# Performance work log

Measured on AMD Instinct MI355X. Metric: run time of the kernel, lower is better.

The kernel has to match this reference:

```python
import jax, jax.numpy as jnp
import numpy as np

EPS = 1e-5


def _linear(x, w, b):
    # torch Linear: y = x @ w.T + b, w shape [out, in]
    return x @ w.T + b


def _batchnorm(x, gamma, beta):
    # training-mode BatchNorm1d: per-feature batch stats, biased variance
    m = jnp.mean(x, axis=0)
    v = jnp.var(x, axis=0)
    return (x - m) * jax.lax.rsqrt(v + EPS) * gamma + beta


def _noise_like(key, x):
    # mimics: mean = x.mean().item(); std = x.std().item() * U(1,2);
    # noise ~ N(mean, std) of x.shape, detached.
    ku, kn = jax.random.split(key)
    m = jax.lax.stop_gradient(jnp.mean(x))
    s = jax.lax.stop_gradient(jnp.std(x, ddof=1))
    u = jax.random.uniform(ku, (), dtype=x.dtype, minval=1.0, maxval=2.0)
    return m + s * u * jax.random.normal(kn, x.shape, dtype=x.dtype)


def setup_inputs() -> dict:
    key = jax.random.key(0)
    ks = jax.random.split(key, 12)
    B = 65536
    x = jax.random.normal(ks[0], (B, 784), dtype=jnp.float32)

    def lin_init(kw, kb, fan_in, fan_out):
        bound = 1.0 / np.sqrt(fan_in)
        w = jax.random.uniform(kw, (fan_out, fan_in), minval=-bound, maxval=bound, dtype=jnp.float32)
        b = jax.random.uniform(kb, (fan_out,), minval=-bound, maxval=bound, dtype=jnp.float32)
        return w, b

    w1, b1 = lin_init(ks[1], ks[2], 784, 48)
    w2, b2 = lin_init(ks[3], ks[4], 48, 24)
    w3, b3 = lin_init(ks[5], ks[6], 24, 10)
    return {
        "x": x,
        "w1": w1, "b1": b1,
        "gamma1": jnp.ones((48,), jnp.float32), "beta1": jnp.zeros((48,), jnp.float32),
        "w2": w2, "b2": b2,
        "gamma2": jnp.ones((24,), jnp.float32), "beta2": jnp.zeros((24,), jnp.float32),
        "w3": w3, "b3": b3,
    }


def reference(x, w1, b1, gamma1, beta1, w2, b2, gamma2, beta2, w3, b3):
    k1 = jax.random.key(1234)
    k2 = jax.random.key(5678)
    h = _batchnorm(_linear(x, w1, b1), gamma1, beta1)
    h = h + _noise_like(k1, h)
    h = jax.nn.relu(h)
    h = _batchnorm(_linear(h, w2, b2), gamma2, beta2)
    h = h + _noise_like(k2, h)
    h = jax.nn.relu(h)
    return _linear(h, w3, b3)
```

## Files before the change

kernel.cpp:

```cpp
#include <hip/hip_runtime.h>
#include <cstdint>
#include <cstring>


constexpr int MROWS = 65536;
constexpr int KDIM  = 784;
constexpr int KPAD  = 800;
constexpr int F1 = 48, F2 = 24, F3 = 10;

using frag_ab = __attribute__((ext_vector_type(8))) short;
using frag_cd = __attribute__((ext_vector_type(4))) float;

union UB { uint4 u; frag_ab f; };

__device__ __forceinline__ uint32_t rotl32(uint32_t v, int r) {
  return (v << r) | (v >> (32 - r));
}

__device__ __forceinline__ uint32_t tf_mix(uint32_t k0, uint32_t k1, uint32_t ctr) {
  uint32_t ks2 = k0 ^ k1 ^ 0x1BD11BDAu;
  uint32_t x0 = k0;
  uint32_t x1 = ctr + k1;
#define TFR(r) { x0 += x1; x1 = rotl32(x1, r); x1 ^= x0; }
  TFR(13) TFR(15) TFR(26) TFR(6)
  x0 += k1;  x1 += ks2 + 1u;
  TFR(17) TFR(29) TFR(16) TFR(24)
  x0 += ks2; x1 += k0 + 2u;
  TFR(13) TFR(15) TFR(26) TFR(6)
  x0 += k0;  x1 += k1 + 3u;
  TFR(17) TFR(29) TFR(16) TFR(24)
  x0 += k1;  x1 += ks2 + 4u;
  TFR(13) TFR(15) TFR(26) TFR(6)
  x0 += ks2; x1 += k0 + 5u;
#undef TFR
  return x0 ^ x1;
}

__device__ __forceinline__ float erfinv_f32(float x) {
  float t = fmaxf(1.0f - x * x, 1.0e-30f);
  float w = -__logf(t);
  float p;
  if (w < 5.0f) {
    w = w - 2.5f;
    p = 2.81022636e-08f;
    p = fmaf(p, w, 3.43273939e-07f);
    p = fmaf(p, w, -3.5233877e-06f);
    p = fmaf(p, w, -4.39150654e-06f);
    p = fmaf(p, w, 0.00021858087f);
    p = fmaf(p, w, -0.00125372503f);
    p = fmaf(p, w, -0.00417768164f);
    p = fmaf(p, w, 0.246640727f);
    p = fmaf(p, w, 1.50140941f);
  } else {
    w = sqrtf(w) - 3.0f;
    p = -0.000200214257f;
    p = fmaf(p, w, 0.000100950558f);
    p = fmaf(p, w, 0.00134934322f);
    p = fmaf(p, w, -0.00367342844f);
    p = fmaf(p, w, 0.00573950773f);
    p = fmaf(p, w, -0.0076224613f);
    p = fmaf(p, w, 0.00943887047f);
    p = fmaf(p, w, 1.00167406f);
    p = fmaf(p, w, 2.83297682f);
  }
  return p * x;
}

__device__ __forceinline__ float noise_normal(uint32_t k0, uint32_t k1, uint32_t ctr) {
  uint32_t bits = tf_mix(k0, k1, ctr);
  float f = __uint_as_float((bits >> 9) | 0x3f800000u) - 1.0f;
  const float lo = -0.99999994f;
  float u = fmaxf(lo, f * 2.0f + lo);
  return 1.41421356f * erfinv_f32(u);
}

__device__ __forceinline__ uint32_t pkbf(float a, float b) {
  uint32_t ua = __float_as_uint(a); ua += 0x7fffu + ((ua >> 16) & 1u);
  uint32_t ub = __float_as_uint(b); ub += 0x7fffu + ((ub >> 16) & 1u);
  return (ua >> 16) | (ub & 0xffff0000u);
}

__device__ __forceinline__ uint32_t cvtpk(float a, float b) {
  uint32_t r;
  asm("v_cvt_pk_bf16_f32 %0, %1, %2" : "=v"(r) : "v"(a), "v"(b));
  return r;
}

__global__ void k_prep(const float* __restrict__ w1, ushort* __restrict__ wb1,
                       float* __restrict__ st) {
  int i = blockIdx.x * 256 + threadIdx.x;
  if (i < 2048) st[i] = 0.f;
  if (i >= F1 * KPAD) return;
  int n = i / KPAD, k = i - n * KPAD;
  float v = (k < KDIM) ? w1[n * KDIM + k] : 0.f;
  uint32_t u = __float_as_uint(v);
  u += 0x7fffu + ((u >> 16) & 1u);
  wb1[i] = (ushort)(u >> 16);
}

__global__ __launch_bounds__(256, 4) void k_gemm1(
    const float* __restrict__ x, const ushort* __restrict__ wb1,
    const float* __restrict__ b1, float* __restrict__ h1,
    float* __restrict__ fsum, float* __restrict__ fssq) {
  __shared__ float reds[4][48], redq[4][48];

  const int t = threadIdx.x;
  const int w = t >> 6;
  const int l = t & 63;
  const int lane16 = l & 15;
  const int quad = l >> 4;
  const int rowbase = blockIdx.x * 64;
  const int myrow = rowbase + w * 16 + lane16;

  frag_cd acc[3];
#pragma unroll
  for (int ct = 0; ct < 3; ++ct)
#pragma unroll
    for (int r = 0; r < 4; ++r) acc[ct][r] = 0.f;

  const float* ap = x + (size_t)myrow * KDIM + quad * 8;
  const ushort* bp0 = wb1 + (size_t)(0 * 16 + lane16) * KPAD + quad * 8;
  const ushort* bp1 = wb1 + (size_t)(1 * 16 + lane16) * KPAD + quad * 8;
  const ushort* bp2 = wb1 + (size_t)(2 * 16 + lane16) * KPAD + quad * 8;

  float4 ca0 = *(const float4*)(ap);
  float4 ca1 = *(const float4*)(ap + 4);
  uint4 cb0 = *(const uint4*)(bp0);
  uint4 cb1 = *(const uint4*)(bp1);
  uint4 cb2 = *(const uint4*)(bp2);

  for (int s = 0; s < 25; ++s) {
    float4 na0 = make_float4(0.f, 0.f, 0.f, 0.f);
    float4 na1 = na0;
    uint4 nb0 = make_uint4(0, 0, 0, 0), nb1 = nb0, nb2 = nb0;
    if (s < 24) {
      const int ko = (s + 1) * 32;
      if (ko + quad * 8 + 8 <= KDIM) {
        na0 = *(const float4*)(ap + ko);
        na1 = *(const float4*)(ap + ko + 4);
      }
      nb0 = *(const uint4*)(bp0 + ko);
      nb1 = *(const uint4*)(bp1 + ko);
      nb2 = *(const uint4*)(bp2 + ko);
    }
    UB a;
    a.u.x = cvtpk(ca0.x, ca0.y);
    a.u.y = cvtpk(ca0.z, ca0.w);
    a.u.z = cvtpk(ca1.x, ca1.y);
    a.u.w = cvtpk(ca1.z, ca1.w);
    UB b;
    b.u = cb0; acc[0] = __builtin_amdgcn_mfma_f32_16x16x32_bf16(a.f, b.f, acc[0], 0, 0, 0);
    b.u = cb1; acc[1] = __builtin_amdgcn_mfma_f32_16x16x32_bf16(a.f, b.f, acc[1], 0, 0, 0);
    b.u = cb2; acc[2] = __builtin_amdgcn_mfma_f32_16x16x32_bf16(a.f, b.f, acc[2], 0, 0, 0);
    ca0 = na0; ca1 = na1; cb0 = nb0; cb1 = nb1; cb2 = nb2;
  }

  float bias[3];
#pragma unroll
  for (int ct = 0; ct < 3; ++ct) bias[ct] = b1[ct * 16 + lane16];
  float psum[3] = {0.f, 0.f, 0.f}, pssq[3] = {0.f, 0.f, 0.f};
#pragma unroll
  for (int r = 0; r < 4; ++r) {
    const int grow = rowbase + w * 16 + quad * 4 + r;
#pragma unroll
    for (int ct = 0; ct < 3; ++ct) {
      float v = acc[ct][r] + bias[ct];
      h1[(size_t)grow * F1 + ct * 16 + lane16] = v;
      psum[ct] += v;
      pssq[ct] += v * v;
    }
  }
#pragma unroll
  for (int ct = 0; ct < 3; ++ct) {
    psum[ct] += __shfl_xor(psum[ct], 16, 64);
    psum[ct] += __shfl_xor(psum[ct], 32, 64);
    pssq[ct] += __shfl_xor(pssq[ct], 16, 64);
    pssq[ct] += __shfl_xor(pssq[ct], 32, 64);
  }
  if (quad == 0) {
#pragma unroll
    for (int ct = 0; ct < 3; ++ct) {
      reds[w][ct * 16 + lane16] = psum[ct];
      redq[w][ct * 16 + lane16] = pssq[ct];
    }
  }
  __syncthreads();
  if (t < F1) {
    float s = reds[0][t] + reds[1][t] + reds[2][t] + reds[3][t];
    float q = redq[0][t] + redq[1][t] + redq[2][t] + redq[3][t];
    const int rep = blockIdx.x & 7;
    atomicAdd(&fsum[rep * 48 + t], s);
    atomicAdd(&fssq[rep * 48 + t], q);
  }
}

__global__ __launch_bounds__(256) void k_layer2(
    const float* __restrict__ h1, const float* __restrict__ w2,
    const float* __restrict__ b2, const float* __restrict__ gamma1,
    const float* __restrict__ beta1, const float* __restrict__ fsum,
    const float* __restrict__ fssq, float u1,
    float* __restrict__ h2, float* __restrict__ fsum2, float* __restrict__ fssq2,
    uint32_t kna, uint32_t knb) {
  __shared__ float a1s[64][49];
  __shared__ float w2s[48][25];
  __shared__ float h2s[64][25];
  __shared__ float bnp[4][48];
  __shared__ float scal[2];

  const int t = threadIdx.x;
  const int rowbase = blockIdx.x * 64;

  float cm = 0.f, cs = 0.f;
  if (t < F1) {
    float s0 = 0.f, q0 = 0.f;
#pragma unroll
    for (int rp = 0; rp < 8; ++rp) { s0 += fsum[rp * 48 + t]; q0 += fssq[rp * 48 + t]; }
    float m = s0 * (1.f / 65536.f);
    float v = q0 * (1.f / 65536.f) - m * m;
    float r = rsqrtf(v + 1e-5f);
    float g = gamma1[t], b = beta1[t];
    bnp[0][t] = m; bnp[1][t] = r; bnp[2][t] = g; bnp[3][t] = b;
    cm = b;
    cs = g * g * r * r * v + b * b;
  }
  if (t < 64) {
#pragma unroll
    for (int off = 32; off > 0; off >>= 1) {
      cm += __shfl_down(cm, off, 64);
      cs += __shfl_down(cs, off, 64);
    }
    if (t == 0) {
      float m = cm / (float)F1;
      float SS = 65536.f * cs;
      float Ntot = 65536.f * (float)F1;
      float s2 = (SS - Ntot * m * m) / (Ntot - 1.f);
      scal[0] = m;
      scal[1] = sqrtf(s2) * u1;
    }
  }
  for (int e = t; e < F2 * 48; e += 256) {
    int c = e / 48, k = e - c * 48;
    w2s[k][c] = w2[e];
  }
  __syncthreads();
  const float m1 = scal[0], su1 = scal[1];

  const int rr = t >> 2;
  const int cc0 = (t & 3) * 12;
  const int grow = rowbase + rr;
  const float* hrow = h1 + (size_t)grow * F1 + cc0;
#pragma unroll
  for (int jj = 0; jj < 12; jj += 4) {
    float4 hv = *(const float4*)(hrow + jj);
    float vv[4] = {hv.x, hv.y, hv.z, hv.w};
#pragma unroll
    for (int q = 0; q < 4; ++q) {
      int c = cc0 + jj + q;
      float bn = (vv[q] - bnp[0][c]) * bnp[1][c] * bnp[2][c] + bnp[3][c];
      uint32_t ctr = (uint32_t)grow * 48u + (uint32_t)c;
      float nz = noise_normal(kna, knb, ctr);
      float val = bn + fmaf(su1, nz, m1);
      a1s[rr][c] = fmaxf(val, 0.f);
    }
  }
  __syncthreads();

  const int rr2 = t & 63;
  const int c0 = (t >> 6) * 6;
  float acc[6] = {0.f, 0.f, 0.f, 0.f, 0.f, 0.f};
#pragma unroll
  for (int k = 0; k < 48; ++k) {
    float a = a1s[rr2][k];
#pragma unroll
    for (int j = 0; j < 6; ++j)
      acc[j] = fmaf(a, w2s[k][c0 + j], acc[j]);
  }
#pragma unroll
  for (int j = 0; j < 6; ++j)
    h2s[rr2][c0 + j] = acc[j] + b2[c0 + j];
  __syncthreads();

  for (int e = t; e < 64 * F2; e += 256) {
    int r2 = e / 24, c2 = e - r2 * 24;
    h2[(size_t)rowbase * F2 + e] = h2s[r2][c2];
  }
  if (t < F2) {
    float s = 0.f, q = 0.f;
    for (int r2 = 0; r2 < 64; ++r2) {
      float v = h2s[r2][t];
      s += v; q += v * v;
    }
    const int rep = blockIdx.x & 7;
    atomicAdd(&fsum2[rep * 24 + t], s);
    atomicAdd(&fssq2[rep * 24 + t], q);
  }
}

__global__ __launch_bounds__(256) void k_layer3(
    const float* __restrict__ h2, const float* __restrict__ w3,
    const float* __restrict__ b3, const float* __restrict__ gamma2,
    const float* __restrict__ beta2, const float* __restrict__ fsum2,
    const float* __restrict__ fssq2, float u2,
    float* __restrict__ out, uint32_t kna, uint32_t knb) {
  __shared__ float a2s[64][25];
  __shared__ float w3s[24][10];
  __shared__ float bnp[4][24];
  __shared__ float scal[2];

  const int t = threadIdx.x;
  const int rowbase = blockIdx.x * 64;

  float cm = 0.f, cs = 0.f;
  if (t < F2) {
    float s0 = 0.f, q0 = 0.f;
#pragma unroll
    for (int rp = 0; rp < 8; ++rp) { s0 += fsum2[rp * 24 + t]; q0 += fssq2[rp * 24 + t]; }
    float m = s0 * (1.f / 65536.f);
    float v = q0 * (1.f / 65536.f) - m * m;
    float r = rsqrtf(v + 1e-5f);
    float g = gamma2[t], b = beta2[t];
    bnp[0][t] = m; bnp[1][t] = r; bnp[2][t] = g; bnp[3][t] = b;
    cm = b;
    cs = g * g * r * r * v + b * b;
  }
  if (t < 64) {
#pragma unroll
    for (int off = 32; off > 0; off >>= 1) {
      cm += __shfl_down(cm, off, 64);
      cs += __shfl_down(cs, off, 64);
    }
    if (t == 0) {
      float m = cm / (float)F2;
      float SS = 65536.f * cs;
      float Ntot = 65536.f * (float)F2;
      float s2 = (SS - Ntot * m * m) / (Ntot - 1.f);
      scal[0] = m;
      scal[1] = sqrtf(s2) * u2;
    }
  }
  if (t < F3 * F2) {
    int c = t / 24, k = t - c * 24;
    w3s[k][c] = w3[t];
  }
  __syncthreads();
  const float m2 = scal[0], su2 = scal[1];

  for (int e = t; e < 64 * F2; e += 256) {
    int r = e / 24, c = e - r * 24;
    float v = h2[(size_t)rowbase * F2 + e];
    float bn = (v - bnp[0][c]) * bnp[1][c] * bnp[2][c] + bnp[3][c];
    uint32_t ctr = (uint32_t)(rowbase * F2 + e);
    float nz = noise_normal(kna, knb, ctr);
    float val = bn + fmaf(su2, nz, m2);
    a2s[r][c] = fmaxf(val, 0.f);
  }
  __syncthreads();

  if (t < 128) {
    const int rr = t & 63;
    const int c0 = (t >> 6) * 5;
    float acc[5] = {0.f, 0.f, 0.f, 0.f, 0.f};
#pragma unroll
    for (int k = 0; k < 24; ++k) {
      float a = a2s[rr][k];
#pragma unroll
      for (int j = 0; j < 5; ++j)
        acc[j] = fmaf(a, w3s[k][c0 + j], acc[j]);
    }
    size_t ob = (size_t)(rowbase + rr) * F3 + c0;
#pragma unroll
    for (int j = 0; j < 5; ++j) out[ob + j] = acc[j] + b3[c0 + j];
  }
}

static void host_tf(uint32_t k0, uint32_t k1, uint32_t c0, uint32_t c1,
                    uint32_t& o0, uint32_t& o1) {
  uint32_t ks2 = k0 ^ k1 ^ 0x1BD11BDAu;
  uint32_t x0 = c0 + k0, x1 = c1 + k1;
  auto R = [&](int r) { x0 += x1; x1 = (x1 << r) | (x1 >> (32 - r)); x1 ^= x0; };
  R(13); R(15); R(26); R(6);  x0 += k1;  x1 += ks2 + 1u;
  R(17); R(29); R(16); R(24); x0 += ks2; x1 += k0 + 2u;
  R(13); R(15); R(26); R(6);  x0 += k0;  x1 += k1 + 3u;
  R(17); R(29); R(16); R(24); x0 += k1;  x1 += ks2 + 4u;
  R(13); R(15); R(26); R(6);  x0 += ks2; x1 += k0 + 5u;
  o0 = x0; o1 = x1;
}

static float host_uniform12(uint32_t seed) {
  uint32_t ka, kb, t0, t1;
  host_tf(0u, seed, 0u, 0u, ka, kb);
  host_tf(ka, kb, 0u, 0u, t0, t1);
  uint32_t bits = t0 ^ t1;
  uint32_t fb = (bits >> 9) | 0x3f800000u;
  float f;
  std::memcpy(&f, &fb, 4);
  return f;
}

extern "C" void kernel_launch(void* const* d_in, const int* in_sizes, int n_in,
                              void* d_out, int out_size, void* d_ws, size_t ws_size,
                              hipStream_t stream) {
  (void)in_sizes; (void)n_in; (void)out_size; (void)ws_size;
  const float* x      = (const float*)d_in[0];
  const float* w1     = (const float*)d_in[1];
  const float* b1     = (const float*)d_in[2];
  const float* gamma1 = (const float*)d_in[3];
  const float* beta1  = (const float*)d_in[4];
  const float* w2     = (const float*)d_in[5];
  const float* b2     = (const float*)d_in[6];
  const float* gamma2 = (const float*)d_in[7];
  const float* beta2  = (const float*)d_in[8];
  const float* w3     = (const float*)d_in[9];
  const float* b3     = (const float*)d_in[10];
  float* out = (float*)d_out;

  float* h1 = (float*)d_ws;
  float* h2 = h1 + (size_t)MROWS * F1;
  float* st = h2 + (size_t)MROWS * F2;
  ushort* wb1 = (ushort*)(st + 2048);

  uint32_t kn1a, kn1b, kn2a, kn2b;
  host_tf(0u, 1234u, 0u, 1u, kn1a, kn1b);
  host_tf(0u, 5678u, 0u, 1u, kn2a, kn2b);
  float u1 = host_uniform12(1234u);
  float u2 = host_uniform12(5678u);

  k_prep<<<(F1 * KPAD + 255) / 256, 256, 0, stream>>>(w1, wb1, st);
  k_gemm1<<<MROWS / 64, 256, 0, stream>>>(x, wb1, b1, h1, st + 0, st + 384);
  k_layer2<<<MROWS / 64, 256, 0, stream>>>(h1, w2, b2, gamma1, beta1,
                                           st + 0, st + 384, u1,
                                           h2, st + 768, st + 960, kn1a, kn1b);
  k_layer3<<<MROWS / 64, 256, 0, stream>>>(h2, w3, b3, gamma2, beta2,
                                           st + 768, st + 960, u2,
                                           out, kn2a, kn2b);
}
```

Measured before the change: 78.01 us.

## Stage x tiles through double-buffered swizzled LDS with coalesced loads in GEMM1

GEMM1 previously had each lane load its own strided 32-byte pieces of x directly into MFMA fragments. Now each block cooperatively loads 128-column chunks of x with row-contiguous float4 loads into a double-buffered, XOR-swizzled shared-memory tile, then reads the A fragments from LDS. The 16-column tail is handled separately. The aim is better coalescing of the dominant x read and overlap of global loads with MFMA work, at the cost of 64KB of LDS per block (launch bounds lowered to 2) and extra barriers.

```diff
diff --git a/kernel.cpp b/kernel.cpp
--- a/kernel.cpp
+++ b/kernel.cpp
@@ -7,6 +7,7 @@
 constexpr int KDIM  = 784;
 constexpr int KPAD  = 800;
 constexpr int F1 = 48, F2 = 24, F3 = 10;
+constexpr int NBLK = 1024;
 
 using frag_ab = __attribute__((ext_vector_type(8))) short;
 using frag_cd = __attribute__((ext_vector_type(4))) float;
@@ -74,12 +75,6 @@
   return 1.41421356f * erfinv_f32(u);
 }
 
-__device__ __forceinline__ uint32_t pkbf(float a, float b) {
-  uint32_t ua = __float_as_uint(a); ua += 0x7fffu + ((ua >> 16) & 1u);
-  uint32_t ub = __float_as_uint(b); ub += 0x7fffu + ((ub >> 16) & 1u);
-  return (ua >> 16) | (ub & 0xffff0000u);
-}
-
 __device__ __forceinline__ uint32_t cvtpk(float a, float b) {
   uint32_t r;
   asm("v_cvt_pk_bf16_f32 %0, %1, %2" : "=v"(r) : "v"(a), "v"(b));
@@ -98,10 +93,11 @@
   wb1[i] = (ushort)(u >> 16);
 }
 
-__global__ __launch_bounds__(256, 4) void k_gemm1(
+__global__ __launch_bounds__(256, 2) void k_gemm1(
     const float* __restrict__ x, const ushort* __restrict__ wb1,
     const float* __restrict__ b1, float* __restrict__ h1,
     float* __restrict__ fsum, float* __restrict__ fssq) {
+  __shared__ float xs[2][64 * 128];
   __shared__ float reds[4][48], redq[4][48];
 
   const int t = threadIdx.x;
@@ -112,47 +108,96 @@
   const int rowbase = blockIdx.x * 64;
   const int myrow = rowbase + w * 16 + lane16;
 
+  const int sr = t >> 2;
+  const int sq = t & 3;
+  const float* srcrow = x + (size_t)(rowbase + sr) * KDIM + sq * 32;
+  const int swz = sr & 15;
+
   frag_cd acc[3];
 #pragma unroll
   for (int ct = 0; ct < 3; ++ct)
 #pragma unroll
     for (int r = 0; r < 4; ++r) acc[ct][r] = 0.f;
 
-  const float* ap = x + (size_t)myrow * KDIM + quad * 8;
   const ushort* bp0 = wb1 + (size_t)(0 * 16 + lane16) * KPAD + quad * 8;
   const ushort* bp1 = wb1 + (size_t)(1 * 16 + lane16) * KPAD + quad * 8;
   const ushort* bp2 = wb1 + (size_t)(2 * 16 + lane16) * KPAD + quad * 8;
 
-  float4 ca0 = *(const float4*)(ap);
-  float4 ca1 = *(const float4*)(ap + 4);
-  uint4 cb0 = *(const uint4*)(bp0);
-  uint4 cb1 = *(const uint4*)(bp1);
-  uint4 cb2 = *(const uint4*)(bp2);
-
-  for (int s = 0; s < 25; ++s) {
-    float4 na0 = make_float4(0.f, 0.f, 0.f, 0.f);
-    float4 na1 = na0;
-    uint4 nb0 = make_uint4(0, 0, 0, 0), nb1 = nb0, nb2 = nb0;
-    if (s < 24) {
-      const int ko = (s + 1) * 32;
-      if (ko + quad * 8 + 8 <= KDIM) {
-        na0 = *(const float4*)(ap + ko);
-        na1 = *(const float4*)(ap + ko + 4);
+  const int ardbase = (w * 16 + lane16) * 128;
+
+  {
+    float4 stg[8];
+#pragma unroll
+    for (int j = 0; j < 8; ++j) stg[j] = *(const float4*)(srcrow + j * 4);
+#pragma unroll
+    for (int j = 0; j < 8; ++j) {
+      int sp = sq * 8 + j;
+      *(float4*)&xs[0][sr * 128 + ((sp ^ swz) << 2)] = stg[j];
+    }
+  }
+  __syncthreads();
+
+  int buf = 0;
+  for (int c = 0; c < 6; ++c) {
+    uint4 b0[4], b1[4], b2[4];
+#pragma unroll
+    for (int ks = 0; ks < 4; ++ks) {
+      const int ko = c * 128 + ks * 32;
+      b0[ks] = *(const uint4*)(bp0 + ko);
+      b1[ks] = *(const uint4*)(bp1 + ko);
+      b2[ks] = *(const uint4*)(bp2 + ko);
+    }
+    float4 stg[8];
+    if (c < 5) {
+#pragma unroll
+      for (int j = 0; j < 8; ++j)
+        stg[j] = *(const float4*)(srcrow + (c + 1) * 128 + j * 4);
+    }
+#pragma unroll
+    for (int ks = 0; ks < 4; ++ks) {
+      const int sp0 = ks * 8 + quad * 2;
+      float4 a0 = *(const float4*)&xs[buf][ardbase + ((sp0 ^ lane16) << 2)];
+      float4 a1 = *(const float4*)&xs[buf][ardbase + (((sp0 + 1) ^ lane16) << 2)];
+      UB a;
+      a.u.x = cvtpk(a0.x, a0.y);
+      a.u.y = cvtpk(a0.z, a0.w);
+      a.u.z = cvtpk(a1.x, a1.y);
+      a.u.w = cvtpk(a1.z, a1.w);
+      UB b;
+      b.u = b0[ks]; acc[0] = __builtin_amdgcn_mfma_f32_16x16x32_bf16(a.f, b.f, acc[0], 0, 0, 0);
+      b.u = b1[ks]; acc[1] = __builtin_amdgcn_mfma_f32_16x16x32_bf16(a.f, b.f, acc[1], 0, 0, 0);
+      b.u = b2[ks]; acc[2] = __builtin_amdgcn_mfma_f32_16x16x32_bf16(a.f, b.f, acc[2], 0, 0, 0);
+    }
+    if (c < 5) {
+#pragma unroll
+      for (int j = 0; j < 8; ++j) {
+        int sp = sq * 8 + j;
+        *(float4*)&xs[buf ^ 1][sr * 128 + ((sp ^ swz) << 2)] = stg[j];
       }
-      nb0 = *(const uint4*)(bp0 + ko);
-      nb1 = *(const uint4*)(bp1 + ko);
-      nb2 = *(const uint4*)(bp2 + ko);
-    }
+    }
+    __syncthreads();
+    buf ^= 1;
+  }
+
+  {
+    float4 a0 = make_float4(0.f, 0.f, 0.f, 0.f), a1 = a0;
+    if (quad < 2) {
+      const float* apt = x + (size_t)myrow * KDIM + 768 + quad * 8;
+      a0 = *(const float4*)(apt);
+      a1 = *(const float4*)(apt + 4);
+    }
+    uint4 tb0 = *(const uint4*)(bp0 + 768);
+    uint4 tb1 = *(const uint4*)(bp1 + 768);
+    uint4 tb2 = *(const uint4*)(bp2 + 768);
     UB a;
-    a.u.x = cvtpk(ca0.x, ca0.y);
-    a.u.y = cvtpk(ca0.z, ca0.w);
-    a.u.z = cvtpk(ca1.x, ca1.y);
-    a.u.w = cvtpk(ca1.z, ca1.w);
+    a.u.x = cvtpk(a0.x, a0.y);
+    a.u.y = cvtpk(a0.z, a0.w);
+    a.u.z = cvtpk(a1.x, a1.y);
+    a.u.w = cvtpk(a1.z, a1.w);
     UB b;
-    b.u = cb0; acc[0] = __builtin_amdgcn_mfma_f32_16x16x32_bf16(a.f, b.f, acc[0], 0, 0, 0);
-    b.u = cb1; acc[1] = __builtin_amdgcn_mfma_f32_16x16x32_bf16(a.f, b.f, acc[1], 0, 0, 0);
-    b.u = cb2; acc[2] = __builtin_amdgcn_mfma_f32_16x16x32_bf16(a.f, b.f, acc[2], 0, 0, 0);
-    ca0 = na0; ca1 = na1; cb0 = nb0; cb1 = nb1; cb2 = nb2;
+    b.u = tb0; acc[0] = __builtin_amdgcn_mfma_f32_16x16x32_bf16(a.f, b.f, acc[0], 0, 0, 0);
+    b.u = tb1; acc[1] = __builtin_amdgcn_mfma_f32_16x16x32_bf16(a.f, b.f, acc[1], 0, 0, 0);
+    b.u = tb2; acc[2] = __builtin_amdgcn_mfma_f32_16x16x32_bf16(a.f, b.f, acc[2], 0, 0, 0);
   }
 
   float bias[3];
@@ -426,11 +471,11 @@
   float u2 = host_uniform12(5678u);
 
   k_prep<<<(F1 * KPAD + 255) / 256, 256, 0, stream>>>(w1, wb1, st);
-  k_gemm1<<<MROWS / 64, 256, 0, stream>>>(x, wb1, b1, h1, st + 0, st + 384);
-  k_layer2<<<MROWS / 64, 256, 0, stream>>>(h1, w2, b2, gamma1, beta1,
-                                           st + 0, st + 384, u1,
-                                           h2, st + 768, st + 960, kn1a, kn1b);
-  k_layer3<<<MROWS / 64, 256, 0, stream>>>(h2, w3, b3, gamma2, beta2,
-                                           st + 768, st + 960, u2,
-                                           out, kn2a, kn2b);
-}
+  k_gemm1<<<NBLK, 256, 0, stream>>>(x, wb1, b1, h1, st + 0, st + 384);
+  k_layer2<<<NBLK, 256, 0, stream>>>(h1, w2, b2, gamma1, beta1,
+                                     st + 0, st + 384, u1,
+                                     h2, st + 768, st + 960, kn1a, kn1b);
+  k_layer3<<<NBLK, 256, 0, stream>>>(h2, w3, b3, gamma2, beta2,
+                                     st + 768, st + 960, u2,
+                                     out, kn2a, kn2b);
+}
```

After: 83.12 us. 1.07x slower.

## Stage x tiles through LDS with coalesced loads and drop the weight-prep kernel

Applied to the files above, without the earlier changes.

The first GEMM now loads x with row-contiguous float4 loads: 16 lanes cover 64 consecutive floats of one row. The data goes into a double-buffered LDS tile, from which each lane reads its MFMA A-fragment, replacing strided per-lane row loads straight from global memory. The separate k_prep kernel that converted w1 to padded bf16 is removed, so each block reads fp32 w1 directly and packs it to bf16 in the loop, with a dedicated tail step for the last 16 columns. Stat buffers are now zeroed with hipMemsetAsync. This trades one launch and better x coalescing for redundant weight conversion work in every block and more LDS traffic.

```diff
diff --git a/kernel.cpp b/kernel.cpp
--- a/kernel.cpp
+++ b/kernel.cpp
@@ -5,8 +5,8 @@
 
 constexpr int MROWS = 65536;
 constexpr int KDIM  = 784;
-constexpr int KPAD  = 800;
 constexpr int F1 = 48, F2 = 24, F3 = 10;
+constexpr int NBLK = 1024;
 
 using frag_ab = __attribute__((ext_vector_type(8))) short;
 using frag_cd = __attribute__((ext_vector_type(4))) float;
@@ -74,34 +74,26 @@
   return 1.41421356f * erfinv_f32(u);
 }
 
-__device__ __forceinline__ uint32_t pkbf(float a, float b) {
-  uint32_t ua = __float_as_uint(a); ua += 0x7fffu + ((ua >> 16) & 1u);
-  uint32_t ub = __float_as_uint(b); ub += 0x7fffu + ((ub >> 16) & 1u);
-  return (ua >> 16) | (ub & 0xffff0000u);
-}
-
 __device__ __forceinline__ uint32_t cvtpk(float a, float b) {
   uint32_t r;
   asm("v_cvt_pk_bf16_f32 %0, %1, %2" : "=v"(r) : "v"(a), "v"(b));
   return r;
 }
 
-__global__ void k_prep(const float* __restrict__ w1, ushort* __restrict__ wb1,
-                       float* __restrict__ st) {
-  int i = blockIdx.x * 256 + threadIdx.x;
-  if (i < 2048) st[i] = 0.f;
-  if (i >= F1 * KPAD) return;
-  int n = i / KPAD, k = i - n * KPAD;
-  float v = (k < KDIM) ? w1[n * KDIM + k] : 0.f;
-  uint32_t u = __float_as_uint(v);
-  u += 0x7fffu + ((u >> 16) & 1u);
-  wb1[i] = (ushort)(u >> 16);
+__device__ __forceinline__ frag_ab packfrag(float4 a0, float4 a1) {
+  UB a;
+  a.u.x = cvtpk(a0.x, a0.y);
+  a.u.y = cvtpk(a0.z, a0.w);
+  a.u.z = cvtpk(a1.x, a1.y);
+  a.u.w = cvtpk(a1.z, a1.w);
+  return a.f;
 }
 
 __global__ __launch_bounds__(256, 4) void k_gemm1(
-    const float* __restrict__ x, const ushort* __restrict__ wb1,
+    const float* __restrict__ x, const float* __restrict__ w1,
     const float* __restrict__ b1, float* __restrict__ h1,
     float* __restrict__ fsum, float* __restrict__ fssq) {
+  __shared__ float xs[2][64][68];
   __shared__ float reds[4][48], redq[4][48];
 
   const int t = threadIdx.x;
@@ -118,41 +110,85 @@
 #pragma unroll
     for (int r = 0; r < 4; ++r) acc[ct][r] = 0.f;
 
-  const float* ap = x + (size_t)myrow * KDIM + quad * 8;
-  const ushort* bp0 = wb1 + (size_t)(0 * 16 + lane16) * KPAD + quad * 8;
-  const ushort* bp1 = wb1 + (size_t)(1 * 16 + lane16) * KPAD + quad * 8;
-  const ushort* bp2 = wb1 + (size_t)(2 * 16 + lane16) * KPAD + quad * 8;
-
-  float4 ca0 = *(const float4*)(ap);
-  float4 ca1 = *(const float4*)(ap + 4);
-  uint4 cb0 = *(const uint4*)(bp0);
-  uint4 cb1 = *(const uint4*)(bp1);
-  uint4 cb2 = *(const uint4*)(bp2);
-
-  for (int s = 0; s < 25; ++s) {
-    float4 na0 = make_float4(0.f, 0.f, 0.f, 0.f);
-    float4 na1 = na0;
-    uint4 nb0 = make_uint4(0, 0, 0, 0), nb1 = nb0, nb2 = nb0;
-    if (s < 24) {
-      const int ko = (s + 1) * 32;
-      if (ko + quad * 8 + 8 <= KDIM) {
-        na0 = *(const float4*)(ap + ko);
-        na1 = *(const float4*)(ap + ko + 4);
-      }
-      nb0 = *(const uint4*)(bp0 + ko);
-      nb1 = *(const uint4*)(bp1 + ko);
-      nb2 = *(const uint4*)(bp2 + ko);
-    }
-    UB a;
-    a.u.x = cvtpk(ca0.x, ca0.y);
-    a.u.y = cvtpk(ca0.z, ca0.w);
-    a.u.z = cvtpk(ca1.x, ca1.y);
-    a.u.w = cvtpk(ca1.z, ca1.w);
-    UB b;
-    b.u = cb0; acc[0] = __builtin_amdgcn_mfma_f32_16x16x32_bf16(a.f, b.f, acc[0], 0, 0, 0);
-    b.u = cb1; acc[1] = __builtin_amdgcn_mfma_f32_16x16x32_bf16(a.f, b.f, acc[1], 0, 0, 0);
-    b.u = cb2; acc[2] = __builtin_amdgcn_mfma_f32_16x16x32_bf16(a.f, b.f, acc[2], 0, 0, 0);
-    ca0 = na0; ca1 = na1; cb0 = nb0; cb1 = nb1; cb2 = nb2;
+  const int sro = (l >> 4);
+  const int scol = (l & 15) * 4;
+  const float* sbase = x + (size_t)(rowbase + w * 16 + sro) * KDIM + scol;
+  const int lrow = w * 16 + sro;
+
+  const float* wp0 = w1 + (size_t)lane16 * KDIM + quad * 8;
+  const float* wp1 = wp0 + (size_t)16 * KDIM;
+  const float* wp2 = wp0 + (size_t)32 * KDIM;
+
+  const float* arow = &xs[0][w * 16 + lane16][0];
+  const int xsstride = 64 * 68;
+
+  float4 sg0, sg1, sg2, sg3;
+
+  sg0 = *(const float4*)(sbase);
+  sg1 = *(const float4*)(sbase + 4 * KDIM);
+  sg2 = *(const float4*)(sbase + 8 * KDIM);
+  sg3 = *(const float4*)(sbase + 12 * KDIM);
+  *(float4*)&xs[0][lrow][scol] = sg0;
+  *(float4*)&xs[0][lrow + 4][scol] = sg1;
+  *(float4*)&xs[0][lrow + 8][scol] = sg2;
+  *(float4*)&xs[0][lrow + 12][scol] = sg3;
+
+#define MFMA_STEP(bufidx, koff)                                                 \
+  {                                                                             \
+    float4 b0a = *(const float4*)(wp0 + (koff));                                \
+    float4 b0b = *(const float4*)(wp0 + (koff) + 4);                            \
+    float4 b1a = *(const float4*)(wp1 + (koff));                                \
+    float4 b1b = *(const float4*)(wp1 + (koff) + 4);                            \
+    float4 b2a = *(const float4*)(wp2 + (koff));                                \
+    float4 b2b = *(const float4*)(wp2 + (koff) + 4);                            \
+    const float* ar = arow + (bufidx) * xsstride + ((koff) & 63) + quad * 8;    \
+    float4 a0 = *(const float4*)(ar);                                           \
+    float4 a1 = *(const float4*)(ar + 4);                                       \
+    frag_ab af = packfrag(a0, a1);                                              \
+    acc[0] = __builtin_amdgcn_mfma_f32_16x16x32_bf16(af, packfrag(b0a, b0b), acc[0], 0, 0, 0); \
+    acc[1] = __builtin_amdgcn_mfma_f32_16x16x32_bf16(af, packfrag(b1a, b1b), acc[1], 0, 0, 0); \
+    acc[2] = __builtin_amdgcn_mfma_f32_16x16x32_bf16(af, packfrag(b2a, b2b), acc[2], 0, 0, 0); \
+  }
+
+  int buf = 0;
+  for (int c = 0; c < 11; ++c) {
+    const int cn = (c + 1) * 64;
+    sg0 = *(const float4*)(sbase + cn);
+    sg1 = *(const float4*)(sbase + cn + 4 * KDIM);
+    sg2 = *(const float4*)(sbase + cn + 8 * KDIM);
+    sg3 = *(const float4*)(sbase + cn + 12 * KDIM);
+    MFMA_STEP(buf, c * 64)
+    MFMA_STEP(buf, c * 64 + 32)
+    *(float4*)&xs[buf ^ 1][lrow][scol] = sg0;
+    *(float4*)&xs[buf ^ 1][lrow + 4][scol] = sg1;
+    *(float4*)&xs[buf ^ 1][lrow + 8][scol] = sg2;
+    *(float4*)&xs[buf ^ 1][lrow + 12][scol] = sg3;
+    buf ^= 1;
+  }
+  float4 ta0 = make_float4(0.f, 0.f, 0.f, 0.f), ta1 = ta0;
+  if (quad < 2) {
+    const float* apt = x + (size_t)myrow * KDIM + 768 + quad * 8;
+    ta0 = *(const float4*)(apt);
+    ta1 = *(const float4*)(apt + 4);
+  }
+  MFMA_STEP(buf, 11 * 64)
+  MFMA_STEP(buf, 11 * 64 + 32)
+#undef MFMA_STEP
+  {
+    float4 b0a = ta0, b0b = ta0, b1a = ta0, b1b = ta0, b2a = ta0, b2b = ta0;
+    b0a = b0b = b1a = b1b = b2a = b2b = make_float4(0.f, 0.f, 0.f, 0.f);
+    if (quad < 2) {
+      b0a = *(const float4*)(wp0 + 768);
+      b0b = *(const float4*)(wp0 + 772);
+      b1a = *(const float4*)(wp1 + 768);
+      b1b = *(const float4*)(wp1 + 772);
+      b2a = *(const float4*)(wp2 + 768);
+      b2b = *(const float4*)(wp2 + 772);
+    }
+    frag_ab af = packfrag(ta0, ta1);
+    acc[0] = __builtin_amdgcn_mfma_f32_16x16x32_bf16(af, packfrag(b0a, b0b), acc[0], 0, 0, 0);
+    acc[1] = __builtin_amdgcn_mfma_f32_16x16x32_bf16(af, packfrag(b1a, b1b), acc[1], 0, 0, 0);
+    acc[2] = __builtin_amdgcn_mfma_f32_16x16x32_bf16(af, packfrag(b2a, b2b), acc[2], 0, 0, 0);
   }
 
   float bias[3];
@@ -417,7 +453,6 @@
   float* h1 = (float*)d_ws;
   float* h2 = h1 + (size_t)MROWS * F1;
   float* st = h2 + (size_t)MROWS * F2;
-  ushort* wb1 = (ushort*)(st + 2048);
 
   uint32_t kn1a, kn1b, kn2a, kn2b;
   host_tf(0u, 1234u, 0u, 1u, kn1a, kn1b);
@@ -425,12 +460,12 @@
   float u1 = host_uniform12(1234u);
   float u2 = host_uniform12(5678u);
 
-  k_prep<<<(F1 * KPAD + 255) / 256, 256, 0, stream>>>(w1, wb1, st);
-  k_gemm1<<<MROWS / 64, 256, 0, stream>>>(x, wb1, b1, h1, st + 0, st + 384);
-  k_layer2<<<MROWS / 64, 256, 0, stream>>>(h1, w2, b2, gamma1, beta1,
-                                           st + 0, st + 384, u1,
-                                           h2, st + 768, st + 960, kn1a, kn1b);
-  k_layer3<<<MROWS / 64, 256, 0, stream>>>(h2, w3, b3, gamma2, beta2,
-                                           st + 768, st + 960, u2,
-                                           out, kn2a, kn2b);
-}
+  hipMemsetAsync(st, 0, 2048 * sizeof(float), stream);
+  k_gemm1<<<NBLK, 256, 0, stream>>>(x, w1, b1, h1, st + 0, st + 384);
+  k_layer2<<<NBLK, 256, 0, stream>>>(h1, w2, b2, gamma1, beta1,
+                                     st + 0, st + 384, u1,
+                                     h2, st + 768, st + 960, kn1a, kn1b);
+  k_layer3<<<NBLK, 256, 0, stream>>>(h2, w3, b3, gamma2, beta2,
+                                     st + 768, st + 960, u2,
+                                     out, kn2a, kn2b);
+}
```

Result: slower. 91.95 us (+17.9%).

## Stage x tiles through double-buffered LDS with coalesced loads in GEMM1

Applied to the files above, without the earlier changes.

GEMM1 now loads contiguous 64-column strips of x per wave with fully coalesced float4 reads. It writes them into a padded, double-buffered shared-memory tile and reads MFMA A-fragments from LDS, while prefetching the next strip and the weight fragments. The 16-column tail is handled separately from global memory. This removes the strided per-lane row reads of the old loop, at the cost of extra LDS traffic and more registers. It relies on intra-wave ordering rather than barriers.

```diff
diff --git a/kernel.cpp b/kernel.cpp
--- a/kernel.cpp
+++ b/kernel.cpp
@@ -7,6 +7,8 @@
 constexpr int KDIM  = 784;
 constexpr int KPAD  = 800;
 constexpr int F1 = 48, F2 = 24, F3 = 10;
+constexpr int NBLK = 1024;
+constexpr int XP   = 68;
 
 using frag_ab = __attribute__((ext_vector_type(8))) short;
 using frag_cd = __attribute__((ext_vector_type(4))) float;
@@ -74,16 +76,19 @@
   return 1.41421356f * erfinv_f32(u);
 }
 
-__device__ __forceinline__ uint32_t pkbf(float a, float b) {
-  uint32_t ua = __float_as_uint(a); ua += 0x7fffu + ((ua >> 16) & 1u);
-  uint32_t ub = __float_as_uint(b); ub += 0x7fffu + ((ub >> 16) & 1u);
-  return (ua >> 16) | (ub & 0xffff0000u);
-}
-
 __device__ __forceinline__ uint32_t cvtpk(float a, float b) {
   uint32_t r;
   asm("v_cvt_pk_bf16_f32 %0, %1, %2" : "=v"(r) : "v"(a), "v"(b));
   return r;
+}
+
+__device__ __forceinline__ frag_ab packfrag(float4 a0, float4 a1) {
+  UB a;
+  a.u.x = cvtpk(a0.x, a0.y);
+  a.u.y = cvtpk(a0.z, a0.w);
+  a.u.z = cvtpk(a1.x, a1.y);
+  a.u.w = cvtpk(a1.z, a1.w);
+  return a.f;
 }
 
 __global__ void k_prep(const float* __restrict__ w1, ushort* __restrict__ wb1,
@@ -102,6 +107,7 @@
     const float* __restrict__ x, const ushort* __restrict__ wb1,
     const float* __restrict__ b1, float* __restrict__ h1,
     float* __restrict__ fsum, float* __restrict__ fssq) {
+  __shared__ float xs[2][64][XP];
   __shared__ float reds[4][48], redq[4][48];
 
   const int t = threadIdx.x;
@@ -118,42 +124,108 @@
 #pragma unroll
     for (int r = 0; r < 4; ++r) acc[ct][r] = 0.f;
 
-  const float* ap = x + (size_t)myrow * KDIM + quad * 8;
-  const ushort* bp0 = wb1 + (size_t)(0 * 16 + lane16) * KPAD + quad * 8;
-  const ushort* bp1 = wb1 + (size_t)(1 * 16 + lane16) * KPAD + quad * 8;
-  const ushort* bp2 = wb1 + (size_t)(2 * 16 + lane16) * KPAD + quad * 8;
-
-  float4 ca0 = *(const float4*)(ap);
-  float4 ca1 = *(const float4*)(ap + 4);
-  uint4 cb0 = *(const uint4*)(bp0);
-  uint4 cb1 = *(const uint4*)(bp1);
-  uint4 cb2 = *(const uint4*)(bp2);
-
-  for (int s = 0; s < 25; ++s) {
-    float4 na0 = make_float4(0.f, 0.f, 0.f, 0.f);
-    float4 na1 = na0;
-    uint4 nb0 = make_uint4(0, 0, 0, 0), nb1 = nb0, nb2 = nb0;
-    if (s < 24) {
-      const int ko = (s + 1) * 32;
-      if (ko + quad * 8 + 8 <= KDIM) {
-        na0 = *(const float4*)(ap + ko);
-        na1 = *(const float4*)(ap + ko + 4);
-      }
-      nb0 = *(const uint4*)(bp0 + ko);
-      nb1 = *(const uint4*)(bp1 + ko);
-      nb2 = *(const uint4*)(bp2 + ko);
-    }
-    UB a;
-    a.u.x = cvtpk(ca0.x, ca0.y);
-    a.u.y = cvtpk(ca0.z, ca0.w);
-    a.u.z = cvtpk(ca1.x, ca1.y);
-    a.u.w = cvtpk(ca1.z, ca1.w);
+  const int sro = l >> 4;
+  const int scol = (l & 15) * 4;
+  const float* sbase = x + (size_t)(rowbase + w * 16 + sro) * KDIM + scol;
+  float* lw0 = &xs[0][w * 16 + sro][scol];
+  float* lw1 = &xs[1][w * 16 + sro][scol];
+
+  const ushort* bp0 = wb1 + (size_t)lane16 * KPAD + quad * 8;
+  const ushort* bp1 = bp0 + 16 * KPAD;
+  const ushort* bp2 = bp0 + 32 * KPAD;
+
+  const float* ar0 = &xs[0][w * 16 + lane16][quad * 8];
+  const float* ar1 = &xs[1][w * 16 + lane16][quad * 8];
+
+#define LOADC(R0, R1, R2, R3, ko)                                \
+  {                                                              \
+    R0 = *(const float4*)(sbase + (ko));                         \
+    R1 = *(const float4*)(sbase + (ko) + 4 * KDIM);              \
+    R2 = *(const float4*)(sbase + (ko) + 8 * KDIM);              \
+    R3 = *(const float4*)(sbase + (ko) + 12 * KDIM);             \
+  }
+#define WRITEC(DST, R0, R1, R2, R3)                              \
+  {                                                              \
+    *(float4*)((DST)) = R0;                                      \
+    *(float4*)((DST) + 4 * XP) = R1;                             \
+    *(float4*)((DST) + 8 * XP) = R2;                             \
+    *(float4*)((DST) + 12 * XP) = R3;                            \
+  }
+#define COMPUTE2(AR, Q0, Q1, Q2, Q3, Q4, Q5)                                      \
+  {                                                                               \
+    frag_ab af = packfrag(*(const float4*)(AR), *(const float4*)((AR) + 4));      \
+    UB b;                                                                         \
+    b.u = Q0; acc[0] = __builtin_amdgcn_mfma_f32_16x16x32_bf16(af, b.f, acc[0], 0, 0, 0); \
+    b.u = Q1; acc[1] = __builtin_amdgcn_mfma_f32_16x16x32_bf16(af, b.f, acc[1], 0, 0, 0); \
+    b.u = Q2; acc[2] = __builtin_amdgcn_mfma_f32_16x16x32_bf16(af, b.f, acc[2], 0, 0, 0); \
+    af = packfrag(*(const float4*)((AR) + 32), *(const float4*)((AR) + 36));      \
+    b.u = Q3; acc[0] = __builtin_amdgcn_mfma_f32_16x16x32_bf16(af, b.f, acc[0], 0, 0, 0); \
+    b.u = Q4; acc[1] = __builtin_amdgcn_mfma_f32_16x16x32_bf16(af, b.f, acc[1], 0, 0, 0); \
+    b.u = Q5; acc[2] = __builtin_amdgcn_mfma_f32_16x16x32_bf16(af, b.f, acc[2], 0, 0, 0); \
+  }
+
+  float4 rA0, rA1, rA2, rA3, rB0, rB1, rB2, rB3;
+
+  LOADC(rA0, rA1, rA2, rA3, 0)
+  LOADC(rB0, rB1, rB2, rB3, 64)
+  float4 ta0 = make_float4(0.f, 0.f, 0.f, 0.f), ta1 = ta0;
+  if (quad < 2) {
+    const float* apt = x + (size_t)myrow * KDIM + 768 + quad * 8;
+    ta0 = *(const float4*)(apt);
+    ta1 = *(const float4*)(apt + 4);
+  }
+  WRITEC(lw0, rA0, rA1, rA2, rA3)
+
+  for (int c = 0; c < 10; c += 2) {
+    uint4 e0 = *(const uint4*)(bp0 + c * 64);
+    uint4 e1 = *(const uint4*)(bp1 + c * 64);
+    uint4 e2 = *(const uint4*)(bp2 + c * 64);
+    uint4 e3 = *(const uint4*)(bp0 + c * 64 + 32);
+    uint4 e4 = *(const uint4*)(bp1 + c * 64 + 32);
+    uint4 e5 = *(const uint4*)(bp2 + c * 64 + 32);
+    LOADC(rA0, rA1, rA2, rA3, (c + 2) * 64)
+    COMPUTE2(ar0, e0, e1, e2, e3, e4, e5)
+    WRITEC(lw1, rB0, rB1, rB2, rB3)
+    uint4 o0 = *(const uint4*)(bp0 + (c + 1) * 64);
+    uint4 o1 = *(const uint4*)(bp1 + (c + 1) * 64);
+    uint4 o2 = *(const uint4*)(bp2 + (c + 1) * 64);
+    uint4 o3 = *(const uint4*)(bp0 + (c + 1) * 64 + 32);
+    uint4 o4 = *(const uint4*)(bp1 + (c + 1) * 64 + 32);
+    uint4 o5 = *(const uint4*)(bp2 + (c + 1) * 64 + 32);
+    LOADC(rB0, rB1, rB2, rB3, (c + 3) * 64)
+    COMPUTE2(ar1, o0, o1, o2, o3, o4, o5)
+    WRITEC(lw0, rA0, rA1, rA2, rA3)
+  }
+  {
+    uint4 e0 = *(const uint4*)(bp0 + 640);
+    uint4 e1 = *(const uint4*)(bp1 + 640);
+    uint4 e2 = *(const uint4*)(bp2 + 640);
+    uint4 e3 = *(const uint4*)(bp0 + 672);
+    uint4 e4 = *(const uint4*)(bp1 + 672);
+    uint4 e5 = *(const uint4*)(bp2 + 672);
+    COMPUTE2(ar0, e0, e1, e2, e3, e4, e5)
+    WRITEC(lw1, rB0, rB1, rB2, rB3)
+    uint4 o0 = *(const uint4*)(bp0 + 704);
+    uint4 o1 = *(const uint4*)(bp1 + 704);
+    uint4 o2 = *(const uint4*)(bp2 + 704);
+    uint4 o3 = *(const uint4*)(bp0 + 736);
+    uint4 o4 = *(const uint4*)(bp1 + 736);
+    uint4 o5 = *(const uint4*)(bp2 + 736);
+    COMPUTE2(ar1, o0, o1, o2, o3, o4, o5)
+  }
+  {
+    uint4 t0 = *(const uint4*)(bp0 + 768);
+    uint4 t1 = *(const uint4*)(bp1 + 768);
+    uint4 t2 = *(const uint4*)(bp2 + 768);
+    frag_ab af = packfrag(ta0, ta1);
     UB b;
-    b.u = cb0; acc[0] = __builtin_amdgcn_mfma_f32_16x16x32_bf16(a.f, b.f, acc[0], 0, 0, 0);
-    b.u = cb1; acc[1] = __builtin_amdgcn_mfma_f32_16x16x32_bf16(a.f, b.f, acc[1], 0, 0, 0);
-    b.u = cb2; acc[2] = __builtin_amdgcn_mfma_f32_16x16x32_bf16(a.f, b.f, acc[2], 0, 0, 0);
-    ca0 = na0; ca1 = na1; cb0 = nb0; cb1 = nb1; cb2 = nb2;
-  }
+    b.u = t0; acc[0] = __builtin_amdgcn_mfma_f32_16x16x32_bf16(af, b.f, acc[0], 0, 0, 0);
+    b.u = t1; acc[1] = __builtin_amdgcn_mfma_f32_16x16x32_bf16(af, b.f, acc[1], 0, 0, 0);
+    b.u = t2; acc[2] = __builtin_amdgcn_mfma_f32_16x16x32_bf16(af, b.f, acc[2], 0, 0, 0);
+  }
+#undef LOADC
+#undef WRITEC
+#undef COMPUTE2
 
   float bias[3];
 #pragma unroll
@@ -426,11 +498,11 @@
   float u2 = host_uniform12(5678u);
 
   k_prep<<<(F1 * KPAD + 255) / 256, 256, 0, stream>>>(w1, wb1, st);
-  k_gemm1<<<MROWS / 64, 256, 0, stream>>>(x, wb1, b1, h1, st + 0, st + 384);
-  k_layer2<<<MROWS / 64, 256, 0, stream>>>(h1, w2, b2, gamma1, beta1,
-                                           st + 0, st + 384, u1,
-                                           h2, st + 768, st + 960, kn1a, kn1b);
-  k_layer3<<<MROWS / 64, 256, 0, stream>>>(h2, w3, b3, gamma2, beta2,
-                                           st + 768, st + 960, u2,
-                                           out, kn2a, kn2b);
-}
+  k_gemm1<<<NBLK, 256, 0, stream>>>(x, wb1, b1, h1, st + 0, st + 384);
+  k_layer2<<<NBLK, 256, 0, stream>>>(h1, w2, b2, gamma1, beta1,
+                                     st + 0, st + 384, u1,
+                                     h2, st + 768, st + 960, kn1a, kn1b);
+  k_layer3<<<NBLK, 256, 0, stream>>>(h2, w3, b3, gamma2, beta2,
+                                     st + 768, st + 960, u2,
+                                     out, kn2a, kn2b);
+}
```

Measured after the change: 74.43 us. 1.05x faster.
